# Performance work log

Hardware: AMD Instinct MI355X
Metric: run time of the kernel (lower is better)

The kernel has to match this reference:

```python
import jax, jax.numpy as jnp
import numpy as np

N = 100000      # nodes
E = 1600000     # edges
F_IN = 16       # in_features
H = 64          # hidden_channels (heads=1)
E_DIM = 9       # edge_dim
NEG_SLOPE = 0.2


def setup_inputs() -> dict:
    key = jax.random.key(0)
    ks = jax.random.split(key, 11)
    x = jax.random.normal(ks[0], (N, F_IN), jnp.float32)
    edge_index = jax.random.randint(ks[1], (2, E), 0, N, dtype=jnp.int64)
    edge_attr = jax.random.normal(ks[2], (E, E_DIM), jnp.float32)
    s_in = 1.0 / np.sqrt(F_IN)
    s_e = 1.0 / np.sqrt(E_DIM)
    s_h = 1.0 / np.sqrt(H)
    W = jax.random.uniform(ks[3], (F_IN, H), jnp.float32, -s_in, s_in)        # GATConv.lin
    W_edge = jax.random.uniform(ks[4], (E_DIM, H), jnp.float32, -s_e, s_e)    # GATConv.lin_edge
    att_src = jax.random.normal(ks[5], (H,), jnp.float32) * 0.1
    att_dst = jax.random.normal(ks[6], (H,), jnp.float32) * 0.1
    att_edge = jax.random.normal(ks[7], (H,), jnp.float32) * 0.1
    bias = jnp.zeros((H,), jnp.float32)                                        # GATConv bias
    lin_w = jax.random.uniform(ks[8], (H, 1), jnp.float32, -s_h, s_h)          # self.lin
    lin_b = jnp.zeros((1,), jnp.float32)
    return {"x": x, "edge_attr": edge_attr, "W": W, "W_edge": W_edge,
            "att_src": att_src, "att_dst": att_dst, "att_edge": att_edge,
            "bias": bias, "lin_w": lin_w, "lin_b": lin_b, "edge_index": edge_index}


def _gat_forward(x, edge_attr, W, W_edge, att_src, att_dst, att_edge, bias,
                 lin_w, lin_b, edge_index):
    n = x.shape[0]
    src, dst = edge_index[0], edge_index[1]
    h = x @ W                                   # [N, H]
    a_src = h @ att_src                         # [N]
    a_dst = h @ att_dst                         # [N]
    # add_self_loops with fill_value='mean': per-node mean of incoming edge_attr
    ones = jnp.ones((src.shape[0],), x.dtype)
    deg = jax.ops.segment_sum(ones, dst, num_segments=n)
    loop_attr = jax.ops.segment_sum(edge_attr, dst, num_segments=n) / jnp.maximum(deg, 1.0)[:, None]
    loops = jnp.arange(n, dtype=src.dtype)
    src_f = jnp.concatenate([src, loops])       # [E+N]
    dst_f = jnp.concatenate([dst, loops])
    ea_f = jnp.concatenate([edge_attr, loop_attr], axis=0)
    a_edge = (ea_f @ W_edge) @ att_edge         # [E+N]
    alpha = a_src[src_f] + a_dst[dst_f] + a_edge
    alpha = jnp.where(alpha >= 0, alpha, NEG_SLOPE * alpha)  # leaky_relu
    # segment softmax over destination nodes (every node has a self-loop -> no empty segments)
    amax = jax.ops.segment_max(alpha, dst_f, num_segments=n)
    ex = jnp.exp(alpha - amax[dst_f])
    denom = jax.ops.segment_sum(ex, dst_f, num_segments=n)
    alpha = ex / (denom[dst_f] + 1e-16)
    msg = h[src_f] * alpha[:, None]             # [E+N, H]
    out_nodes = jax.ops.segment_sum(msg, dst_f, num_segments=n) + bias
    x2 = jax.nn.relu(out_nodes)
    # edge readout on the ORIGINAL edge list
    pair = (x2[src] + x2[dst]) * 0.5            # [E, H]
    return jax.nn.sigmoid(pair @ lin_w + lin_b) # [E, 1]


def reference(x, edge_attr, W, W_edge, att_src, att_dst, att_edge, bias,
              lin_w, lin_b, edge_index):
    return _gat_forward(x, edge_attr, W, W_edge, att_src, att_dst, att_edge,
                        bias, lin_w, lin_b, edge_index)
```

## Files before the change

### kernel.cpp

```cpp
#include <hip/hip_runtime.h>
#include <hip/hip_bf16.h>
#include <math.h>

#define N_NODES 100000
#define N_EDGES 1600000
#define F_IN 16
#define HDIM 64
#define E_DIM 9
#define NEG 0.2f

#define CAP 64
#define NSLICE 8
#define SLICE_W 12500
#define PART_BLOCKS 1024
#define PART_STRIDE ((PART_BLOCKS / NSLICE) * 256)
#define FIXSCALE 16777216.0f

typedef unsigned long long ull;
typedef long long ll;

__global__ __launch_bounds__(256) void k_node_h(
    const float* __restrict__ x, const float* __restrict__ W,
    const float* __restrict__ att_src, const float* __restrict__ att_dst,
    __hip_bfloat16* __restrict__ hbf, float* __restrict__ a_src,
    float* __restrict__ a_dst) {
  __shared__ float sW[F_IN * HDIM];
  int t = threadIdx.x;
  for (int i = t; i < F_IN * HDIM; i += 256) sW[i] = W[i];
  __syncthreads();
  int lane = t & 63;
  int node = blockIdx.x * 4 + (t >> 6);
  if (node >= N_NODES) return;
  const float* xr = x + node * F_IN;
  float acc = 0.f;
#pragma unroll
  for (int k = 0; k < F_IN; ++k) acc += xr[k] * sW[k * HDIM + lane];
  hbf[(size_t)node * HDIM + lane] = __float2bfloat16(acc);
  float v1 = acc * att_src[lane];
  float v2 = acc * att_dst[lane];
#pragma unroll
  for (int off = 32; off > 0; off >>= 1) {
    v1 += __shfl_down(v1, off);
    v2 += __shfl_down(v2, off);
  }
  if (lane == 0) { a_src[node] = v1; a_dst[node] = v2; }
}

__global__ void k_we(const float* __restrict__ W_edge,
                     const float* __restrict__ att_edge, float* __restrict__ w_e) {
  int d = threadIdx.x;
  if (d < E_DIM) {
    float s = 0.f;
    for (int hh = 0; hh < HDIM; ++hh) s += W_edge[d * HDIM + hh] * att_edge[hh];
    w_e[d] = s;
  }
}

__global__ __launch_bounds__(256) void k_edge_pre(
    const float* __restrict__ ea, const int* __restrict__ ei,
    const float* __restrict__ w_e, const float* __restrict__ a_src,
    const float* __restrict__ a_dst, unsigned* __restrict__ epack,
    float* __restrict__ aebuf) {
  __shared__ float swe[E_DIM];
  if (threadIdx.x < E_DIM) swe[threadIdx.x] = w_e[threadIdx.x];
  __syncthreads();
  int e = blockIdx.x * 256 + threadIdx.x;
  if (e >= N_EDGES) return;
  int s = __builtin_nontemporal_load(ei + e);
  int d = __builtin_nontemporal_load(ei + N_EDGES + e);
  float a_e = 0.f;
#pragma unroll
  for (int k = 0; k < E_DIM; ++k)
    a_e += __builtin_nontemporal_load(ea + (size_t)e * E_DIM + k) * swe[k];
  float al = a_src[s] + a_dst[d] + a_e;
  al = al >= 0.f ? al : NEG * al;
  float ee = expf(al);
  unsigned b = __float_as_uint(ee);
  b += 0x7fffu + ((b >> 16) & 1u);
  unsigned pk = ((unsigned)s << 15) | ((b >> 16) & 0x7fffu);
  __builtin_nontemporal_store(pk, epack + e);
  __builtin_nontemporal_store(a_e, aebuf + e);
}

__global__ __launch_bounds__(256) void k_part(
    const int* __restrict__ ei, const unsigned* __restrict__ epack,
    const float* __restrict__ aebuf, ull* __restrict__ packed,
    unsigned* __restrict__ bpack) {
  int t = threadIdx.x;
  int slice = blockIdx.x & (NSLICE - 1);
  int j = blockIdx.x >> 3;
  int lo = slice * SLICE_W;
  for (int e = j * 256 + t; e < N_EDGES; e += PART_STRIDE) {
    int d = ei[N_EDGES + e];
    unsigned r = (unsigned)(d - lo);
    if (r < SLICE_W) {
      unsigned pk = epack[e];
      float ae = aebuf[e];
      ll q = (ll)lrintf(ae * FIXSCALE);
      ull old = atomicAdd(packed + d, ((ull)q << 20) | 1ull);
      unsigned pos = (unsigned)(old & 0xFFFFFu);
      if (pos < CAP) bpack[(size_t)d * CAP + pos] = pk;
    }
  }
}

__global__ __launch_bounds__(256) void k_gather(
    const ull* __restrict__ packed, const unsigned* __restrict__ bpack,
    const __hip_bfloat16* __restrict__ hbf, const float* __restrict__ a_src,
    const float* __restrict__ a_dst, const float* __restrict__ bias,
    const float* __restrict__ lin_w, float* __restrict__ s_node) {
  int t = threadIdx.x;
  int lane = t & 63;
  int node = blockIdx.x * 4 + (t >> 6);
  if (node >= N_NODES) return;
  ull p = packed[node];
  unsigned deg = (unsigned)(p & 0xFFFFFu);
  float sumae = (float)((double)((ll)p >> 20) * (1.0 / (double)FIXSCALE));
  const unsigned* row = bpack + (size_t)node * CAP;
  float acc = 0.f, denom = 0.f;
  unsigned k = 0;
  for (; k + 4 <= deg; k += 4) {
    uint4 p4 = *(const uint4*)(row + k);
    float e0 = __uint_as_float((p4.x & 0x7fffu) << 16);
    float e1 = __uint_as_float((p4.y & 0x7fffu) << 16);
    float e2 = __uint_as_float((p4.z & 0x7fffu) << 16);
    float e3 = __uint_as_float((p4.w & 0x7fffu) << 16);
    float h0 = __bfloat162float(hbf[(size_t)(p4.x >> 15) * HDIM + lane]);
    float h1 = __bfloat162float(hbf[(size_t)(p4.y >> 15) * HDIM + lane]);
    float h2 = __bfloat162float(hbf[(size_t)(p4.z >> 15) * HDIM + lane]);
    float h3 = __bfloat162float(hbf[(size_t)(p4.w >> 15) * HDIM + lane]);
    denom += (e0 + e1) + (e2 + e3);
    acc += e0 * h0 + e1 * h1 + e2 * h2 + e3 * h3;
  }
  for (; k < deg; ++k) {
    unsigned pe = row[k];
    float ee = __uint_as_float((pe & 0x7fffu) << 16);
    denom += ee;
    acc += ee * __bfloat162float(hbf[(size_t)(pe >> 15) * HDIM + lane]);
  }
  float cnt = (float)deg;
  float all = a_src[node] + a_dst[node] + sumae / fmaxf(cnt, 1.f);
  all = all >= 0.f ? all : NEG * all;
  float eel = expf(all);
  denom += eel;
  acc += eel * __bfloat162float(hbf[(size_t)node * HDIM + lane]);
  float o = fmaxf(acc / (denom + 1e-16f) + bias[lane], 0.f) * lin_w[lane];
#pragma unroll
  for (int off = 32; off > 0; off >>= 1) o += __shfl_down(o, off);
  if (lane == 0) s_node[node] = o;
}

__global__ __launch_bounds__(256) void k_out(
    const int* __restrict__ ei, const float* __restrict__ s_node,
    const float* __restrict__ lin_b, float* __restrict__ out) {
  int e = blockIdx.x * 256 + threadIdx.x;
  if (e >= N_EDGES) return;
  int s = __builtin_nontemporal_load(ei + e);
  int d = __builtin_nontemporal_load(ei + N_EDGES + e);
  float z = 0.5f * (s_node[s] + s_node[d]) + lin_b[0];
  float r = 1.f / (1.f + expf(-z));
  __builtin_nontemporal_store(r, out + e);
}

extern "C" void kernel_launch(void* const* d_in, const int* in_sizes, int n_in,
                              void* d_out, int out_size, void* d_ws, size_t ws_size,
                              hipStream_t stream) {
  const float* x        = (const float*)d_in[0];
  const float* edge_attr= (const float*)d_in[1];
  const float* W        = (const float*)d_in[2];
  const float* W_edge   = (const float*)d_in[3];
  const float* att_src  = (const float*)d_in[4];
  const float* att_dst  = (const float*)d_in[5];
  const float* att_edge = (const float*)d_in[6];
  const float* bias     = (const float*)d_in[7];
  const float* lin_w    = (const float*)d_in[8];
  const float* lin_b    = (const float*)d_in[9];
  const int*   ei       = (const int*)d_in[10];
  float* out = (float*)d_out;

  char* base = (char*)d_ws;
  __hip_bfloat16* hbf = (__hip_bfloat16*)base;
  unsigned* epack = (unsigned*)(base + (size_t)N_NODES * HDIM * 2);
  float*    aebuf = (float*)(epack + N_EDGES);
  unsigned* bpack = (unsigned*)(aebuf + N_EDGES);
  ull*      packed= (ull*)(bpack + (size_t)N_NODES * CAP);
  float* a_src  = (float*)(packed + N_NODES);
  float* a_dst  = a_src + N_NODES;
  float* s_node = a_dst + N_NODES;
  float* w_e    = s_node + N_NODES;

  hipMemsetAsync(packed, 0, sizeof(ull) * N_NODES, stream);

  int nb_node   = (N_NODES + 3) / 4;
  int nb_edge_t = (N_EDGES + 255) / 256;

  k_node_h  <<<nb_node, 256, 0, stream>>>(x, W, att_src, att_dst, hbf, a_src, a_dst);
  k_we      <<<1, 64, 0, stream>>>(W_edge, att_edge, w_e);
  k_edge_pre<<<nb_edge_t, 256, 0, stream>>>(edge_attr, ei, w_e, a_src, a_dst,
                                            epack, aebuf);
  k_part    <<<PART_BLOCKS, 256, 0, stream>>>(ei, epack, aebuf, packed, bpack);
  k_gather  <<<nb_node, 256, 0, stream>>>(packed, bpack, hbf, a_src, a_dst,
                                          bias, lin_w, s_node);
  k_out     <<<nb_edge_t, 256, 0, stream>>>(ei, s_node, lin_b, out);
}
```

Before: 392.7 us.

## Pre-bucket edges by destination slice in edge_pre, stream slices in partition

Edge preprocessing now bins each block's edges by destination slice in shared memory and appends packed 64-bit entries (local dst, fp16 edge score, src/exp) to per-slice global streams. The partition kernel then reads only its own slice's stream instead of rescanning every edge's destination for each of 8 slices. This removes the redundant full reads of the edge index, packed-edge and edge-score arrays in the partition pass. The gather loop is also unrolled by 8. The change stores edge scores in fp16, which slightly reduces precision of the self-loop mean. It also relies on a fixed per-slice capacity and an edge count divisible by 256.

```diff
diff --git a/kernel.cpp b/kernel.cpp
--- a/kernel.cpp
+++ b/kernel.cpp
@@ -1,5 +1,6 @@
 #include <hip/hip_runtime.h>
 #include <hip/hip_bf16.h>
+#include <hip/hip_fp16.h>
 #include <math.h>
 
 #define N_NODES 100000
@@ -12,8 +13,8 @@
 #define CAP 64
 #define NSLICE 8
 #define SLICE_W 12500
+#define SLICE_CAP 210000
 #define PART_BLOCKS 1024
-#define PART_STRIDE ((PART_BLOCKS / NSLICE) * 256)
 #define FIXSCALE 16777216.0f
 
 typedef unsigned long long ull;
@@ -59,13 +60,18 @@
 __global__ __launch_bounds__(256) void k_edge_pre(
     const float* __restrict__ ea, const int* __restrict__ ei,
     const float* __restrict__ w_e, const float* __restrict__ a_src,
-    const float* __restrict__ a_dst, unsigned* __restrict__ epack,
-    float* __restrict__ aebuf) {
+    const float* __restrict__ a_dst, ull* __restrict__ sstream,
+    unsigned* __restrict__ gcount) {
   __shared__ float swe[E_DIM];
-  if (threadIdx.x < E_DIM) swe[threadIdx.x] = w_e[threadIdx.x];
-  __syncthreads();
-  int e = blockIdx.x * 256 + threadIdx.x;
-  if (e >= N_EDGES) return;
+  __shared__ unsigned cnt[NSLICE];
+  __shared__ unsigned basex[NSLICE];
+  __shared__ unsigned gbase[NSLICE];
+  __shared__ ull sdata[256];
+  int t = threadIdx.x;
+  if (t < E_DIM) swe[t] = w_e[t];
+  if (t < NSLICE) cnt[t] = 0u;
+  __syncthreads();
+  int e = blockIdx.x * 256 + t;
   int s = __builtin_nontemporal_load(ei + e);
   int d = __builtin_nontemporal_load(ei + N_EDGES + e);
   float a_e = 0.f;
@@ -78,29 +84,47 @@
   unsigned b = __float_as_uint(ee);
   b += 0x7fffu + ((b >> 16) & 1u);
   unsigned pk = ((unsigned)s << 15) | ((b >> 16) & 0x7fffu);
-  __builtin_nontemporal_store(pk, epack + e);
-  __builtin_nontemporal_store(a_e, aebuf + e);
-}
-
-__global__ __launch_bounds__(256) void k_part(
-    const int* __restrict__ ei, const unsigned* __restrict__ epack,
-    const float* __restrict__ aebuf, ull* __restrict__ packed,
-    unsigned* __restrict__ bpack) {
+  unsigned slice = (unsigned)d / SLICE_W;
+  unsigned dloc = (unsigned)d - slice * SLICE_W;
+  unsigned aeh = (unsigned)__half_as_ushort(__float2half(a_e));
+  ull entry = ((ull)dloc << 48) | ((ull)aeh << 32) | (ull)pk;
+  unsigned mypos = atomicAdd(&cnt[slice], 1u);
+  __syncthreads();
+  if (t == 0) {
+    unsigned a = 0;
+    for (int i = 0; i < NSLICE; ++i) { basex[i] = a; a += cnt[i]; }
+  }
+  __syncthreads();
+  if (t < NSLICE) gbase[t] = atomicAdd(gcount + t, cnt[t]);
+  sdata[basex[slice] + mypos] = entry;
+  __syncthreads();
+  unsigned ss = 0;
+#pragma unroll
+  for (int i = 1; i < NSLICE; ++i) ss += (t >= basex[i]) ? 1u : 0u;
+  unsigned off = gbase[ss] + ((unsigned)t - basex[ss]);
+  if (off < SLICE_CAP)
+    __builtin_nontemporal_store(sdata[t], sstream + (size_t)ss * SLICE_CAP + off);
+}
+
+__global__ __launch_bounds__(256) void k_part2(
+    const ull* __restrict__ sstream, const unsigned* __restrict__ gcount,
+    ull* __restrict__ packed, unsigned* __restrict__ bpack) {
   int t = threadIdx.x;
   int slice = blockIdx.x & (NSLICE - 1);
   int j = blockIdx.x >> 3;
+  unsigned n = gcount[slice];
+  const ull* sp = sstream + (size_t)slice * SLICE_CAP;
   int lo = slice * SLICE_W;
-  for (int e = j * 256 + t; e < N_EDGES; e += PART_STRIDE) {
-    int d = ei[N_EDGES + e];
-    unsigned r = (unsigned)(d - lo);
-    if (r < SLICE_W) {
-      unsigned pk = epack[e];
-      float ae = aebuf[e];
-      ll q = (ll)lrintf(ae * FIXSCALE);
-      ull old = atomicAdd(packed + d, ((ull)q << 20) | 1ull);
-      unsigned pos = (unsigned)(old & 0xFFFFFu);
-      if (pos < CAP) bpack[(size_t)d * CAP + pos] = pk;
-    }
+  const unsigned stride = (PART_BLOCKS / NSLICE) * 256;
+  for (unsigned i = (unsigned)j * 256 + t; i < n; i += stride) {
+    ull entry = sp[i];
+    int d = lo + (int)(unsigned)(entry >> 48);
+    float ae = __half2float(__ushort_as_half((unsigned short)((entry >> 32) & 0xFFFFu)));
+    unsigned pk = (unsigned)(entry & 0xFFFFFFFFu);
+    ll q = (ll)lrintf(ae * FIXSCALE);
+    ull old = atomicAdd(packed + d, ((ull)q << 20) | 1ull);
+    unsigned pos = (unsigned)(old & 0xFFFFFu);
+    if (pos < CAP) bpack[(size_t)d * CAP + pos] = pk;
   }
 }
 
@@ -119,6 +143,29 @@
   const unsigned* row = bpack + (size_t)node * CAP;
   float acc = 0.f, denom = 0.f;
   unsigned k = 0;
+  for (; k + 8 <= deg; k += 8) {
+    uint4 pa = *(const uint4*)(row + k);
+    uint4 pb = *(const uint4*)(row + k + 4);
+    float e0 = __uint_as_float((pa.x & 0x7fffu) << 16);
+    float e1 = __uint_as_float((pa.y & 0x7fffu) << 16);
+    float e2 = __uint_as_float((pa.z & 0x7fffu) << 16);
+    float e3 = __uint_as_float((pa.w & 0x7fffu) << 16);
+    float e4 = __uint_as_float((pb.x & 0x7fffu) << 16);
+    float e5 = __uint_as_float((pb.y & 0x7fffu) << 16);
+    float e6 = __uint_as_float((pb.z & 0x7fffu) << 16);
+    float e7 = __uint_as_float((pb.w & 0x7fffu) << 16);
+    float h0 = __bfloat162float(hbf[(size_t)(pa.x >> 15) * HDIM + lane]);
+    float h1 = __bfloat162float(hbf[(size_t)(pa.y >> 15) * HDIM + lane]);
+    float h2 = __bfloat162float(hbf[(size_t)(pa.z >> 15) * HDIM + lane]);
+    float h3 = __bfloat162float(hbf[(size_t)(pa.w >> 15) * HDIM + lane]);
+    float h4 = __bfloat162float(hbf[(size_t)(pb.x >> 15) * HDIM + lane]);
+    float h5 = __bfloat162float(hbf[(size_t)(pb.y >> 15) * HDIM + lane]);
+    float h6 = __bfloat162float(hbf[(size_t)(pb.z >> 15) * HDIM + lane]);
+    float h7 = __bfloat162float(hbf[(size_t)(pb.w >> 15) * HDIM + lane]);
+    denom += ((e0 + e1) + (e2 + e3)) + ((e4 + e5) + (e6 + e7));
+    acc += (e0 * h0 + e1 * h1 + e2 * h2 + e3 * h3)
+         + (e4 * h4 + e5 * h5 + e6 * h6 + e7 * h7);
+  }
   for (; k + 4 <= deg; k += 4) {
     uint4 p4 = *(const uint4*)(row + k);
     float e0 = __uint_as_float((p4.x & 0x7fffu) << 16);
@@ -180,25 +227,25 @@
 
   char* base = (char*)d_ws;
   __hip_bfloat16* hbf = (__hip_bfloat16*)base;
-  unsigned* epack = (unsigned*)(base + (size_t)N_NODES * HDIM * 2);
-  float*    aebuf = (float*)(epack + N_EDGES);
-  unsigned* bpack = (unsigned*)(aebuf + N_EDGES);
-  ull*      packed= (ull*)(bpack + (size_t)N_NODES * CAP);
-  float* a_src  = (float*)(packed + N_NODES);
+  ull* sstream = (ull*)(base + (size_t)N_NODES * HDIM * 2);
+  unsigned* bpack = (unsigned*)(sstream + (size_t)NSLICE * SLICE_CAP);
+  ull* packed = (ull*)(bpack + (size_t)N_NODES * CAP);
+  unsigned* gcount = (unsigned*)(packed + N_NODES);
+  float* a_src  = (float*)(gcount + NSLICE);
   float* a_dst  = a_src + N_NODES;
   float* s_node = a_dst + N_NODES;
   float* w_e    = s_node + N_NODES;
 
-  hipMemsetAsync(packed, 0, sizeof(ull) * N_NODES, stream);
+  hipMemsetAsync(packed, 0, sizeof(ull) * N_NODES + sizeof(unsigned) * NSLICE, stream);
 
   int nb_node   = (N_NODES + 3) / 4;
-  int nb_edge_t = (N_EDGES + 255) / 256;
+  int nb_edge_t = N_EDGES / 256;
 
   k_node_h  <<<nb_node, 256, 0, stream>>>(x, W, att_src, att_dst, hbf, a_src, a_dst);
   k_we      <<<1, 64, 0, stream>>>(W_edge, att_edge, w_e);
   k_edge_pre<<<nb_edge_t, 256, 0, stream>>>(edge_attr, ei, w_e, a_src, a_dst,
-                                            epack, aebuf);
-  k_part    <<<PART_BLOCKS, 256, 0, stream>>>(ei, epack, aebuf, packed, bpack);
+                                            sstream, gcount);
+  k_part2   <<<PART_BLOCKS, 256, 0, stream>>>(sstream, gcount, packed, bpack);
   k_gather  <<<nb_node, 256, 0, stream>>>(packed, bpack, hbf, a_src, a_dst,
                                           bias, lin_w, s_node);
   k_out     <<<nb_edge_t, 256, 0, stream>>>(ei, s_node, lin_b, out);
```

New measurement: 421.6 us. 7.4% more time.
